# Kernel optimization log

Measured on AMD Instinct MI355X. Metric: run time of the kernel, lower is better.

Reference implementation:

```python
import jax, jax.numpy as jnp
import numpy as np

B, N_BOX, NUM_CLASSES = 32, 50, 20
FEATURE_SIZES = np.array([[52, 52], [26, 26], [13, 13]])
NUM_CENG = FEATURE_SIZES[:, 0] * FEATURE_SIZES[:, 1]            # [2704, 676, 169]
NUM_TOTAL = int((NUM_CENG * 3).sum())                            # 10647
ANCS_SCALE = np.array([[10, 13], [16, 30], [33, 23], [30, 61], [62, 45],
                       [59, 119], [116, 90], [156, 198], [373, 326]], dtype=np.float32) / 416.0
NEG_IOU_THRESHOLD = 0.5
NUM_NEG = 1000
EPS = 1e-7

def _build_anchor_grid():
    # rows ordered: level(52,26,13) -> cell (row-major) -> 3 anchors per cell
    out = []
    for lvl in range(3):
        f = int(FEATURE_SIZES[lvl, 0])
        ys, xs = np.meshgrid(np.arange(f), np.arange(f), indexing='ij')
        xy = (np.stack([xs, ys], -1).reshape(-1, 2).astype(np.float32)) / f  # cell corner (col/f,row/f)
        xy3 = np.repeat(xy, 3, axis=0)                                       # [f*f*3, 2]
        wh3 = np.tile(ANCS_SCALE[lvl * 3:(lvl + 1) * 3], (f * f, 1))
        out.append(np.concatenate([xy3, wh3], 1))
    return np.concatenate(out, 0)                                            # [10647, 4]

ANCS = jnp.asarray(_build_anchor_grid())
FSIZES = jnp.asarray(np.repeat(FEATURE_SIZES[:, 0].astype(np.float32), NUM_CENG * 3))  # [10647]
OFF_CENG = jnp.asarray([0.0, 2704.0, 3380.0])   # prefix sums of NUM_CENG
FW_LVL = jnp.asarray([52.0, 26.0, 13.0])


def _xywh2ltrb(xywh):
    return jnp.concatenate([xywh[..., :2] - xywh[..., 2:] * 0.5,
                            xywh[..., :2] + xywh[..., 2:] * 0.5], -1)


def _ciou(a, b):
    # a, b: broadcastable [..., 4] ltrb -> CIoU [...]
    lt = jnp.maximum(a[..., :2], b[..., :2])
    rb = jnp.minimum(a[..., 2:], b[..., 2:])
    wh = jnp.clip(rb - lt, 0.0)
    inter = wh[..., 0] * wh[..., 1]
    wa = a[..., 2] - a[..., 0]; ha = a[..., 3] - a[..., 1]
    wb = b[..., 2] - b[..., 0]; hb = b[..., 3] - b[..., 1]
    union = wa * ha + wb * hb - inter
    iou = inter / (union + EPS)
    clt = jnp.minimum(a[..., :2], b[..., :2])
    crb = jnp.maximum(a[..., 2:], b[..., 2:])
    cwh = crb - clt
    c2 = cwh[..., 0] ** 2 + cwh[..., 1] ** 2 + EPS
    ctr_a = (a[..., :2] + a[..., 2:]) * 0.5
    ctr_b = (b[..., :2] + b[..., 2:]) * 0.5
    rho2 = jnp.sum((ctr_a - ctr_b) ** 2, -1)
    v = (4.0 / (jnp.pi ** 2)) * (jnp.arctan(wa / (ha + EPS)) - jnp.arctan(wb / (hb + EPS))) ** 2
    alpha = jax.lax.stop_gradient(v / (1.0 - iou + v + EPS))
    return iou - rho2 / c2 - alpha * v


def _bce(p, t):
    p = jnp.clip(p, EPS, 1.0 - EPS)
    return -(t * jnp.log(p) + (1.0 - t) * jnp.log(1.0 - p))


def _per_image(p, boxes, labels):
    # p: [10647, 25], boxes: [N,4] ltrb, labels: [N] (1-based)
    N = boxes.shape[0]
    bxy = (boxes[:, :2] + boxes[:, 2:]) * 0.5
    bwh = boxes[:, 2:] - boxes[:, :2]
    # ---- anchor-target matching (source's loop always takes argmax anchor) ----
    p1xy = jnp.repeat(bxy, 9, axis=0)                                       # [N*9, 2]
    fpairs = jnp.repeat(jnp.asarray(FEATURE_SIZES, jnp.float32), 3, axis=0)  # [9, 2]
    p2f = jnp.tile(fpairs, (N, 1))                                          # [N*9, 2]
    colrow = jnp.floor(p1xy * p2f)                                          # (col, row) per box/anchor
    anc_xy = colrow / p2f
    anc_wh = jnp.tile(jnp.asarray(ANCS_SCALE), (N, 1))
    anc_ltrb = _xywh2ltrb(jnp.concatenate([anc_xy, anc_wh], 1))
    ids = jnp.arange(N, dtype=boxes.dtype)
    iou_m = _ciou(boxes[:, None, :] + ids[:, None, None],
                  anc_ltrb[None, :, :] + jnp.repeat(ids, 9)[None, :, None])  # [N, N*9]
    k = jnp.argmax(iou_m, axis=1) % 9                                       # best anchor id 0..8
    lvl = k // 3                                                            # (source quirk: //len(NUMS_ANC))
    cr = colrow[jnp.arange(N) * 9 + k]                                      # [N, 2]
    off_cr = cr[:, 1] * FW_LVL[lvl] + cr[:, 0]
    midx = ((OFF_CENG[lvl] + off_cr) * 3.0 + lvl.astype(jnp.float32)).astype(jnp.int32)  # [N]
    # ---- decode predictions ----
    p_box_xy = p[:, :2] / FSIZES[:, None] + ANCS[:, :2]
    p_box_wh = jnp.exp(p[:, 2:4]) * ANCS[:, 2:]
    p_ltrb = _xywh2ltrb(jnp.concatenate([p_box_xy, p_box_wh], -1))          # [10647, 4]
    # ---- positive losses ----
    pcls = p[midx, 5:]                                                      # [N, C]
    t = jax.nn.one_hot(labels - 1, NUM_CLASSES, dtype=pcls.dtype)
    l_cls = _bce(pcls, t).sum()
    pconf = p[midx, 4]
    l_conf_p = (-jnp.log(jnp.clip(pconf, EPS, 1.0 - EPS))).sum()
    ciou_pos = _ciou(boxes, p_ltrb[midx])                                   # [N]
    w = 2.0 - bwh[:, 0] * bwh[:, 1]
    l_box = (w * (1.0 - ciou_pos)).sum()
    # ---- negative conf loss (replicates filtered-coordinate indexing) ----
    iou_all = _ciou(boxes[:, None, :], p_ltrb[None, :, :])                  # [N, 10647]
    mx = iou_all.max(axis=0)
    mask = mx < NEG_IOU_THRESHOLD
    key = jnp.where(mask, mx, jnp.inf)
    order = jnp.argsort(key)                                                # masked-in first, ascending
    rank = jnp.cumsum(mask) - 1                                             # filtered coordinate per row
    neg_idx = rank[order][:NUM_NEG]                                         # == source's _max_index[:NUM_NEG]
    pneg = p[neg_idx, 4]
    l_conf_n = (-jnp.log(jnp.clip(1.0 - pneg, EPS, 1.0 - EPS))).sum()
    nf = jnp.asarray(N, p.dtype)
    return l_cls / nf, l_box / nf, l_conf_p / nf, l_conf_n


def setup_inputs() -> dict:
    key = jax.random.key(0)
    k1, k2, k3, k4 = jax.random.split(key, 4)
    p_yolo_ts = jax.random.uniform(k1, (B, NUM_TOTAL, 4 + 1 + NUM_CLASSES),
                                   dtype=jnp.float32, minval=1e-4, maxval=1.0 - 1e-4)
    cxy = jax.random.uniform(k2, (B, N_BOX, 2), minval=0.15, maxval=0.85)
    wh = jax.random.uniform(k3, (B, N_BOX, 2), minval=0.05, maxval=0.25)
    boxes = jnp.concatenate([cxy - wh * 0.5, cxy + wh * 0.5], -1).astype(jnp.float32)
    labels = jax.random.randint(k4, (B, N_BOX), 1, NUM_CLASSES + 1, dtype=jnp.int32)
    return {"p_yolo_ts": p_yolo_ts, "boxes": boxes, "labels": labels}


def reference(p_yolo_ts, boxes, labels):
    l_cls, l_box, l_cp, l_cn = jax.vmap(_per_image)(p_yolo_ts, boxes, labels)
    return l_cp.mean() + l_cn.mean() + l_box.mean() + l_cls.mean()
```

## Files before the change

kernel.cpp:

```cpp
#include <hip/hip_runtime.h>

namespace {

constexpr int BB   = 32;
constexpr int NBOX = 50;
constexpr int NCLS = 20;
constexpr int NT   = 10647;
constexpr int NNEG = 1000;
constexpr int DEC_BLOCKS = (NT + 127) / 128;
constexpr int POS_BLOCKS = (NBOX + 3) / 4;
constexpr float EPS = 1e-7f;
constexpr float PI4 = (float)(4.0 / 9.869604401089358);

__device__ __constant__ float c_aw[9] = {10.f/416.f,16.f/416.f,33.f/416.f,30.f/416.f,62.f/416.f,59.f/416.f,116.f/416.f,156.f/416.f,373.f/416.f};
__device__ __constant__ float c_ah[9] = {13.f/416.f,30.f/416.f,23.f/416.f,61.f/416.f,45.f/416.f,119.f/416.f,90.f/416.f,198.f/416.f,326.f/416.f};

__device__ __forceinline__ float fastrcp(float x) {
  return __builtin_amdgcn_rcpf(x);
}

__device__ __forceinline__ float dciou(float al, float at, float ar, float ab,
                                       float bl, float bt, float br, float bb,
                                       float atanA, float atanB) {
  float ltx = fmaxf(al, bl), lty = fmaxf(at, bt);
  float rbx = fminf(ar, br), rby = fminf(ab, bb);
  float wx = fmaxf(rbx - ltx, 0.f), wy = fmaxf(rby - lty, 0.f);
  float inter = wx * wy;
  float wa = ar - al, ha = ab - at;
  float wb = br - bl, hb = bb - bt;
  float uni = wa * ha + wb * hb - inter;
  float iou = inter / (uni + EPS);
  float cw = fmaxf(ar, br) - fminf(al, bl);
  float ch = fmaxf(ab, bb) - fminf(at, bt);
  float c2 = cw * cw + ch * ch + EPS;
  float dx = (al + ar) * 0.5f - (bl + br) * 0.5f;
  float dy = (at + ab) * 0.5f - (bt + bb) * 0.5f;
  float rho2 = dx * dx + dy * dy;
  float dat = atanA - atanB;
  float v = PI4 * (dat * dat);
  float alpha = v / (1.f - iou + v + EPS);
  return iou - rho2 / c2 - alpha * v;
}

__device__ __forceinline__ float dciou_h(float4 A, float4 E,
                                         float bl, float bt, float br, float bb,
                                         float areaB,
                                         float cxb, float cyb, float atanB) {
  float ltx = fmaxf(A.x, bl), lty = fmaxf(A.y, bt);
  float rbx = fminf(A.z, br), rby = fminf(A.w, bb);
  float wx = fmaxf(rbx - ltx, 0.f), wy = fmaxf(rby - lty, 0.f);
  float inter = wx * wy;
  float uni = E.w + areaB - inter;
  float iou = inter * fastrcp(uni + EPS);
  float cw = fmaxf(A.z, br) - fminf(A.x, bl);
  float ch = fmaxf(A.w, bb) - fminf(A.y, bt);
  float c2 = cw * cw + ch * ch + EPS;
  float dx = E.x - cxb;
  float dy = E.y - cyb;
  float rho2 = dx * dx + dy * dy;
  float dat = E.z - atanB;
  float v = PI4 * (dat * dat);
  float alpha = v * fastrcp(1.f - iou + v + EPS);
  return iou - rho2 * fastrcp(c2) - alpha * v;
}

__device__ __forceinline__ int wave_incl_scan(int x, int lane) {
  #pragma unroll
  for (int off = 1; off < 64; off <<= 1) {
    int y = __shfl_up(x, off);
    if (lane >= off) x += y;
  }
  return x;
}

__global__ __launch_bounds__(256, 2) void k_main(const float* __restrict__ p,
                            const float* __restrict__ boxes,
                            const int* __restrict__ labels,
                            unsigned long long* __restrict__ comp,
                            float* __restrict__ pcls, float* __restrict__ pbox,
                            float* __restrict__ pcp, float* __restrict__ out) {
  const int b = blockIdx.y;
  const int tid = threadIdx.x;
  if (blockIdx.x == 0 && b == 0 && tid == 0) out[0] = 0.f;

  if (blockIdx.x < DEC_BLOCKS) {
    __shared__ float4 sA[NBOX];
    __shared__ float4 sE[NBOX];
    if (tid < NBOX) {
      const float* bp = boxes + (b * NBOX + tid) * 4;
      float l = bp[0], t = bp[1], r = bp[2], d = bp[3];
      sA[tid] = make_float4(l, t, r, d);
      float wa = r - l, ha = d - t;
      sE[tid] = make_float4((l + r) * 0.5f, (t + d) * 0.5f,
                            atanf(wa / (ha + EPS)), wa * ha);
    }
    __syncthreads();

    const int par = tid & 1;
    const int j = blockIdx.x * 128 + (tid >> 1);
    if (j >= NT) return;

    int lvl = (j < 8112) ? 0 : ((j < 10140) ? 1 : 2);
    int jb0 = (lvl == 0) ? 0 : ((lvl == 1) ? 8112 : 10140);
    int f   = (lvl == 0) ? 52 : ((lvl == 1) ? 26 : 13);
    int jj = j - jb0;
    int cell = jj / 3, a = jj % 3 + lvl * 3;
    int x = cell % f, y = cell / f;
    float ff = (float)f;
    const float* pr = p + ((size_t)b * NT + j) * 25;
    float px = pr[0] / ff + (float)x / ff;
    float py = pr[1] / ff + (float)y / ff;
    float pw = expf(pr[2]) * c_aw[a];
    float ph = expf(pr[3]) * c_ah[a];
    float bl = px - pw * 0.5f, bt = py - ph * 0.5f;
    float br = px + pw * 0.5f, bbv = py + ph * 0.5f;
    float wb = br - bl, hb = bbv - bt;
    float areab = wb * hb;
    float cxb = (bl + br) * 0.5f, cyb = (bt + bbv) * 0.5f;
    float atb = atanf(wb / (hb + EPS));

    float4 rA[25], rE[25];
    #pragma unroll
    for (int i = 0; i < 25; ++i) {
      rA[i] = sA[2 * i + par];
      rE[i] = sE[2 * i + par];
    }
    float mx0 = -INFINITY, mx1 = -INFINITY;
    #pragma unroll
    for (int i = 0; i + 1 < 25; i += 2) {
      float v0 = dciou_h(rA[i],     rE[i],     bl, bt, br, bbv, areab, cxb, cyb, atb);
      float v1 = dciou_h(rA[i + 1], rE[i + 1], bl, bt, br, bbv, areab, cxb, cyb, atb);
      mx0 = fmaxf(mx0, v0);
      mx1 = fmaxf(mx1, v1);
    }
    mx0 = fmaxf(mx0, dciou_h(rA[24], rE[24], bl, bt, br, bbv, areab, cxb, cyb, atb));
    float mx = fmaxf(mx0, mx1);
    mx = fmaxf(mx, __shfl_xor(mx, 1));

    if (par == 0) {
      float key = (mx < 0.5f) ? mx : INFINITY;
      unsigned int u = __float_as_uint(key);
      u = (u & 0x80000000u) ? ~u : (u | 0x80000000u);
      comp[(size_t)b * NT + j] = ((unsigned long long)u << 14) | (unsigned long long)j;
    }
  } else {
    const int lane = tid & 63;
    const int wave = tid >> 6;
    const int i = (blockIdx.x - DEC_BLOCKS) * 4 + wave;

    __shared__ float scx[NBOX], scy[NBOX];
    if (tid < NBOX) {
      const float* bp = boxes + (b * NBOX + tid) * 4;
      float l = bp[0], t = bp[1], r = bp[2], d = bp[3];
      scx[tid] = (l + r) * 0.5f;
      scy[tid] = (t + d) * 0.5f;
    }
    __syncthreads();
    if (i >= NBOX) return;

    const float* bi = boxes + (b * NBOX + i) * 4;
    float bl0 = bi[0], bt0 = bi[1], br0 = bi[2], bd0 = bi[3];
    float fi = (float)i;
    float al = bl0 + fi, at = bt0 + fi, ar = br0 + fi, ad = bd0 + fi;
    float wa = ar - al, ha = ad - at;
    float atanA = atanf(wa / (ha + EPS));

    float bestv = -INFINITY; int bestm = 1 << 30;
    #pragma unroll
    for (int m = lane; m < 9 * NBOX; m += 64) {
      int jb = m / 9, aa = m % 9;
      float fa = (aa < 3) ? 52.f : (aa < 6 ? 26.f : 13.f);
      float col = floorf(scx[jb] * fa);
      float row = floorf(scy[jb] * fa);
      float ax = col / fa, ay = row / fa;
      float aw = c_aw[aa], ah = c_ah[aa];
      float fj = (float)jb;
      float bl = (ax - aw * 0.5f) + fj;
      float bt = (ay - ah * 0.5f) + fj;
      float br = (ax + aw * 0.5f) + fj;
      float bd = (ay + ah * 0.5f) + fj;
      float wb = br - bl, hb = bd - bt;
      float atanB = atanf(wb / (hb + EPS));
      float v = dciou(al, at, ar, ad, bl, bt, br, bd, atanA, atanB);
      if (v > bestv) { bestv = v; bestm = m; }
    }
    #pragma unroll
    for (int off = 32; off > 0; off >>= 1) {
      float ov = __shfl_down(bestv, off);
      int om = __shfl_down(bestm, off);
      if (ov > bestv || (ov == bestv && om < bestm)) { bestv = ov; bestm = om; }
    }
    int bm = __shfl(bestm, 0);

    int k = bm % 9;
    int lvl = k / 3;
    float fk = (k < 3) ? 52.f : (k < 6 ? 26.f : 13.f);
    float col = floorf(scx[i] * fk);
    float row = floorf(scy[i] * fk);
    float offc = (lvl == 0) ? 0.f : (lvl == 1 ? 2704.f : 3380.f);
    int midx = (int)((offc + row * fk + col) * 3.0f + (float)lvl);

    const float* prm = p + ((size_t)b * NT + midx) * 25;
    int lab = labels[b * NBOX + i] - 1;

    float lc = 0.f;
    if (lane < NCLS) {
      float pc = prm[5 + lane];
      pc = fminf(fmaxf(pc, EPS), 1.f - EPS);
      float tt = (lane == lab) ? 1.f : 0.f;
      lc = -(tt * logf(pc) + (1.f - tt) * logf(1.f - pc));
    }
    #pragma unroll
    for (int off = 32; off > 0; off >>= 1) lc += __shfl_down(lc, off);

    if (lane == 0) {
      pcls[b * NBOX + i] = lc;
      float pc4 = prm[4];
      pc4 = fminf(fmaxf(pc4, EPS), 1.f - EPS);
      pcp[b * NBOX + i] = -logf(pc4);

      int lvl2 = (midx < 8112) ? 0 : ((midx < 10140) ? 1 : 2);
      int jb0 = (lvl2 == 0) ? 0 : ((lvl2 == 1) ? 8112 : 10140);
      int f2  = (lvl2 == 0) ? 52 : ((lvl2 == 1) ? 26 : 13);
      int jj2 = midx - jb0;
      int cell2 = jj2 / 3, a2 = jj2 % 3 + lvl2 * 3;
      int xx = cell2 % f2, yy = cell2 / f2;
      float ff2 = (float)f2;
      float px = prm[0] / ff2 + (float)xx / ff2;
      float py = prm[1] / ff2 + (float)yy / ff2;
      float pw = expf(prm[2]) * c_aw[a2];
      float ph = expf(prm[3]) * c_ah[a2];
      float pbl = px - pw * 0.5f, pbt = py - ph * 0.5f;
      float pbr = px + pw * 0.5f, pbd = py + ph * 0.5f;

      float wb = pbr - pbl, hb = pbd - pbt;
      float atanB = atanf(wb / (hb + EPS));
      float wa0 = br0 - bl0, ha0 = bd0 - bt0;
      float atanA0 = atanf(wa0 / (ha0 + EPS));
      float cp = dciou(bl0, bt0, br0, bd0, pbl, pbt, pbr, pbd, atanA0, atanB);
      float w = 2.f - wa0 * ha0;
      pbox[b * NBOX + i] = w * (1.f - cp);
    }
  }
}

__global__ __launch_bounds__(1024) void k_neg2(const unsigned long long* __restrict__ comp,
                                               const float* __restrict__ p,
                                               const float* __restrict__ pcls,
                                               const float* __restrict__ pbox,
                                               const float* __restrict__ pcp,
                                               float* __restrict__ out) {
  int b = blockIdx.x;
  const unsigned long long* c = comp + (size_t)b * NT;
  const int tid = threadIdx.x, lane = tid & 63, wave = tid >> 6;

  __shared__ int hist[4096];
  __shared__ int s_w[16];
  __shared__ unsigned long long s_pref;
  __shared__ int s_rem;
  __shared__ int s_digit;
  __shared__ int s_rem_next;
  __shared__ int s_csel;
  __shared__ int s_done;
  __shared__ int s_cnt;
  __shared__ float s_facc[16];
  __shared__ float s_lcn;
  __shared__ int s_tot[11][16];
  __shared__ int s_off[11][16];

  unsigned long long v[11];
  #pragma unroll
  for (int k = 0; k < 11; ++k) {
    int j = k * 1024 + tid;
    v[k] = (j < NT) ? c[j] : ~0ull;
  }

  int wincl[11];
  #pragma unroll
  for (int k = 0; k < 11; ++k) {
    unsigned long long x = v[k];
    int flag = ((x >> 14) < 0xFF800000ull) ? 1 : 0;
    int incl = wave_incl_scan(flag, lane);
    wincl[k] = incl;
    if (lane == 63) s_tot[k][wave] = incl;
  }
  __syncthreads();
  if (wave == 0) {
    int i0 = lane * 3;
    int a0 = (i0     < 176) ? s_tot[i0 / 16][i0 % 16] : 0;
    int a1 = (i0 + 1 < 176) ? s_tot[(i0 + 1) / 16][(i0 + 1) % 16] : 0;
    int a2 = (i0 + 2 < 176) ? s_tot[(i0 + 2) / 16][(i0 + 2) % 16] : 0;
    int lsum = a0 + a1 + a2;
    int linc = wave_incl_scan(lsum, lane);
    int lexc = linc - lsum;
    if (i0     < 176) s_off[i0 / 16][i0 % 16] = lexc;
    if (i0 + 1 < 176) s_off[(i0 + 1) / 16][(i0 + 1) % 16] = lexc + a0;
    if (i0 + 2 < 176) s_off[(i0 + 2) / 16][(i0 + 2) % 16] = lexc + a0 + a1;
    if (lane == 63) s_cnt = linc;
  }
  if (tid == 0) { s_pref = 0ull; s_rem = NNEG - 1; s_done = 0; }
  __syncthreads();
  const bool spec = (s_cnt >= NNEG);

  for (int pass = 0; pass < 4; ++pass) {
    if (s_done) break;
    int lo = 36 - pass * 12;
    for (int h = tid; h < 4096; h += 1024) hist[h] = 0;
    __syncthreads();
    unsigned long long pref = s_pref;
    #pragma unroll
    for (int k = 0; k < 11; ++k) {
      unsigned long long x = v[k];
      bool fin = ((x >> 14) < 0xFF800000ull);
      if ((!spec || fin) && (x >> (lo + 12)) == (pref >> (lo + 12)))
        atomicAdd(&hist[(int)((x >> lo) & 4095ull)], 1);
    }
    __syncthreads();
    int base = tid * 4;
    int c0 = hist[base], c1 = hist[base + 1], c2 = hist[base + 2], c3 = hist[base + 3];
    int tsum = c0 + c1 + c2 + c3;
    int incl = wave_incl_scan(tsum, lane);
    if (lane == 63) s_w[wave] = incl;
    __syncthreads();
    if (wave == 0) {
      int wv = (lane < 16) ? s_w[lane] : 0;
      int wincl2 = wave_incl_scan(wv, lane);
      if (lane < 16) s_w[lane] = wincl2 - wv;
    }
    __syncthreads();
    int excl = incl - tsum + s_w[wave];
    int rem = s_rem;
    int p0 = excl, p1 = p0 + c0, p2 = p1 + c1, p3 = p2 + c2;
    if (rem >= p0 && rem < p0 + c0) { s_digit = base + 0; s_rem_next = rem - p0; s_csel = c0; }
    if (rem >= p1 && rem < p1 + c1) { s_digit = base + 1; s_rem_next = rem - p1; s_csel = c1; }
    if (rem >= p2 && rem < p2 + c2) { s_digit = base + 2; s_rem_next = rem - p2; s_csel = c2; }
    if (rem >= p3 && rem < p3 + c3) { s_digit = base + 3; s_rem_next = rem - p3; s_csel = c3; }
    __syncthreads();
    if (tid == 0) {
      s_pref |= ((unsigned long long)s_digit) << lo;
      s_rem = s_rem_next;
      if (s_rem_next == s_csel - 1) {
        s_pref |= (lo > 0) ? ((1ull << lo) - 1ull) : 0ull;
        s_done = 1;
      }
    }
    __syncthreads();
  }
  const unsigned long long T = s_pref;

  float acc = 0.f;
  const float* pb = p + (size_t)b * NT * 25;
  #pragma unroll
  for (int k = 0; k < 11; ++k) {
    unsigned long long x = v[k];
    if (x <= T) {
      int idx = s_off[k][wave] + wincl[k] - 1;
      if (idx < 0) idx += NT;
      float q = 1.f - pb[(size_t)idx * 25 + 4];
      q = fminf(fmaxf(q, EPS), 1.f - EPS);
      acc += -logf(q);
    }
  }

  #pragma unroll
  for (int off = 32; off > 0; off >>= 1) acc += __shfl_down(acc, off);
  if (lane == 0) s_facc[wave] = acc;
  __syncthreads();
  if (tid == 0) {
    float s = 0.f;
    #pragma unroll
    for (int w = 0; w < 16; ++w) s += s_facc[w];
    s_lcn = s;
  }
  __syncthreads();

  if (wave == 0) {
    float s3 = 0.f;
    if (lane < NBOX)
      s3 = pcls[b * NBOX + lane] + pbox[b * NBOX + lane] + pcp[b * NBOX + lane];
    #pragma unroll
    for (int off = 32; off > 0; off >>= 1) s3 += __shfl_down(s3, off);
    if (lane == 0)
      atomicAdd(out, (s3 / (float)NBOX + s_lcn) / (float)BB);
  }
}

}

extern "C" void kernel_launch(void* const* d_in, const int* in_sizes, int n_in,
                              void* d_out, int out_size, void* d_ws, size_t ws_size,
                              hipStream_t stream) {
  const float* p      = (const float*)d_in[0];
  const float* boxes  = (const float*)d_in[1];
  const int*   labels = (const int*)d_in[2];
  float* out = (float*)d_out;

  char* ws = (char*)d_ws;
  size_t off = 0;
  unsigned long long* comp = (unsigned long long*)(ws + off); off += (size_t)BB * NT * sizeof(unsigned long long);
  float* pcls = (float*)(ws + off);                off += BB * NBOX * sizeof(float);
  float* pbox = (float*)(ws + off);                off += BB * NBOX * sizeof(float);
  float* pcp  = (float*)(ws + off);                off += BB * NBOX * sizeof(float);

  dim3 g1(DEC_BLOCKS + POS_BLOCKS, BB);
  k_main<<<g1, 256, 0, stream>>>(p, boxes, labels, comp, pcls, pbox, pcp, out);
  k_neg2<<<BB, 1024, 0, stream>>>(comp, p, pcls, pbox, pcp, out);
}
```

Baseline: 51.92 us.

## Process two anchors per thread pair to reuse shared GT box registers

After: 53.22 us. +2.5%, slower.

```diff
diff --git a/kernel.cpp b/kernel.cpp
--- a/kernel.cpp
+++ b/kernel.cpp
@@ -7,7 +7,7 @@
 constexpr int NCLS = 20;
 constexpr int NT   = 10647;
 constexpr int NNEG = 1000;
-constexpr int DEC_BLOCKS = (NT + 127) / 128;
+constexpr int DEC_BLOCKS = (NT + 255) / 256;
 constexpr int POS_BLOCKS = (NBOX + 3) / 4;
 constexpr float EPS = 1e-7f;
 constexpr float PI4 = (float)(4.0 / 9.869604401089358);
@@ -64,6 +64,30 @@
   return iou - rho2 * fastrcp(c2) - alpha * v;
 }
 
+struct Anc { float bl, bt, br, bb, areab, cxb, cyb, atb; };
+__device__ __forceinline__ Anc decode_anchor(const float* __restrict__ p, int b, int j) {
+  int lvl = (j < 8112) ? 0 : ((j < 10140) ? 1 : 2);
+  int jb0 = (lvl == 0) ? 0 : ((lvl == 1) ? 8112 : 10140);
+  int f   = (lvl == 0) ? 52 : ((lvl == 1) ? 26 : 13);
+  int jj = j - jb0;
+  int cell = jj / 3, a = jj % 3 + lvl * 3;
+  int x = cell % f, y = cell / f;
+  float ff = (float)f;
+  const float* pr = p + ((size_t)b * NT + j) * 25;
+  float px = pr[0] / ff + (float)x / ff;
+  float py = pr[1] / ff + (float)y / ff;
+  float pw = expf(pr[2]) * c_aw[a];
+  float ph = expf(pr[3]) * c_ah[a];
+  Anc o;
+  o.bl = px - pw * 0.5f; o.bt = py - ph * 0.5f;
+  o.br = px + pw * 0.5f; o.bb = py + ph * 0.5f;
+  float wb = o.br - o.bl, hb = o.bb - o.bt;
+  o.areab = wb * hb;
+  o.cxb = (o.bl + o.br) * 0.5f; o.cyb = (o.bt + o.bb) * 0.5f;
+  o.atb = atanf(wb / (hb + EPS));
+  return o;
+}
+
 __device__ __forceinline__ int wave_incl_scan(int x, int lane) {
   #pragma unroll
   for (int off = 1; off < 64; off <<= 1) {
@@ -97,27 +121,15 @@
     __syncthreads();
 
     const int par = tid & 1;
-    const int j = blockIdx.x * 128 + (tid >> 1);
-    if (j >= NT) return;
-
-    int lvl = (j < 8112) ? 0 : ((j < 10140) ? 1 : 2);
-    int jb0 = (lvl == 0) ? 0 : ((lvl == 1) ? 8112 : 10140);
-    int f   = (lvl == 0) ? 52 : ((lvl == 1) ? 26 : 13);
-    int jj = j - jb0;
-    int cell = jj / 3, a = jj % 3 + lvl * 3;
-    int x = cell % f, y = cell / f;
-    float ff = (float)f;
-    const float* pr = p + ((size_t)b * NT + j) * 25;
-    float px = pr[0] / ff + (float)x / ff;
-    float py = pr[1] / ff + (float)y / ff;
-    float pw = expf(pr[2]) * c_aw[a];
-    float ph = expf(pr[3]) * c_ah[a];
-    float bl = px - pw * 0.5f, bt = py - ph * 0.5f;
-    float br = px + pw * 0.5f, bbv = py + ph * 0.5f;
-    float wb = br - bl, hb = bbv - bt;
-    float areab = wb * hb;
-    float cxb = (bl + br) * 0.5f, cyb = (bt + bbv) * 0.5f;
-    float atb = atanf(wb / (hb + EPS));
+    const int pair = tid >> 1;
+    const int j0 = blockIdx.x * 256 + pair;
+    const int j1 = j0 + 128;
+    const bool act0 = (j0 < NT), act1 = (j1 < NT);
+    const int jc0 = act0 ? j0 : (NT - 1);
+    const int jc1 = act1 ? j1 : (NT - 1);
+
+    Anc A0 = decode_anchor(p, b, jc0);
+    Anc A1 = decode_anchor(p, b, jc1);
 
     float4 rA[25], rE[25];
     #pragma unroll
@@ -127,21 +139,28 @@
     }
     float mx0 = -INFINITY, mx1 = -INFINITY;
     #pragma unroll
-    for (int i = 0; i + 1 < 25; i += 2) {
-      float v0 = dciou_h(rA[i],     rE[i],     bl, bt, br, bbv, areab, cxb, cyb, atb);
-      float v1 = dciou_h(rA[i + 1], rE[i + 1], bl, bt, br, bbv, areab, cxb, cyb, atb);
+    for (int i = 0; i < 25; ++i) {
+      float v0 = dciou_h(rA[i], rE[i], A0.bl, A0.bt, A0.br, A0.bb, A0.areab, A0.cxb, A0.cyb, A0.atb);
+      float v1 = dciou_h(rA[i], rE[i], A1.bl, A1.bt, A1.br, A1.bb, A1.areab, A1.cxb, A1.cyb, A1.atb);
       mx0 = fmaxf(mx0, v0);
       mx1 = fmaxf(mx1, v1);
     }
-    mx0 = fmaxf(mx0, dciou_h(rA[24], rE[24], bl, bt, br, bbv, areab, cxb, cyb, atb));
-    float mx = fmaxf(mx0, mx1);
-    mx = fmaxf(mx, __shfl_xor(mx, 1));
+    mx0 = fmaxf(mx0, __shfl_xor(mx0, 1));
+    mx1 = fmaxf(mx1, __shfl_xor(mx1, 1));
 
     if (par == 0) {
-      float key = (mx < 0.5f) ? mx : INFINITY;
-      unsigned int u = __float_as_uint(key);
-      u = (u & 0x80000000u) ? ~u : (u | 0x80000000u);
-      comp[(size_t)b * NT + j] = ((unsigned long long)u << 14) | (unsigned long long)j;
+      if (act0) {
+        float key = (mx0 < 0.5f) ? mx0 : INFINITY;
+        unsigned int u = __float_as_uint(key);
+        u = (u & 0x80000000u) ? ~u : (u | 0x80000000u);
+        comp[(size_t)b * NT + j0] = ((unsigned long long)u << 14) | (unsigned long long)j0;
+      }
+      if (act1) {
+        float key = (mx1 < 0.5f) ? mx1 : INFINITY;
+        unsigned int u = __float_as_uint(key);
+        u = (u & 0x80000000u) ? ~u : (u | 0x80000000u);
+        comp[(size_t)b * NT + j1] = ((unsigned long long)u << 14) | (unsigned long long)j1;
+      }
     }
   } else {
     const int lane = tid & 63;
```
